# Kernel optimization log

Measured on AMD Instinct MI355X. Metric: run time of the kernel, lower is better.

The kernel has to match this reference:

```python
import jax, jax.numpy as jnp
import numpy as np

BATCH, SEQ, D_IN, D_ST = 16, 8192, 64, 128  # in_features=64, out_features(state)=128


def setup_inputs() -> dict:
    key = jax.random.key(0)
    k0, k1, k2, k3 = jax.random.split(key, 4)
    x = jax.random.normal(k0, (BATCH, SEQ, D_IN), dtype=jnp.float32)
    # State-transition matrix A (HiPPO-initialized in the original). We draw a
    # random dense matrix scaled to spectral radius ~0.9 so the 8192-step
    # recurrence stays numerically stable.
    A = jax.random.normal(k1, (D_ST, D_ST), dtype=jnp.float32) * (0.9 / np.sqrt(D_ST))
    Bw = jax.random.normal(k2, (D_ST, D_IN), dtype=jnp.float32) / np.sqrt(D_IN)
    Bb = jnp.zeros((D_ST,), dtype=jnp.float32)  # bias=True on B
    Cw = jax.random.normal(k3, (D_IN, D_ST), dtype=jnp.float32) / np.sqrt(D_ST)
    return {"x": x, "A": A, "Bw": Bw, "Bb": Bb, "Cw": Cw}


def reference(x, A, Bw, Bb, Cw):
    # Discrete linear SSM: h_t = A h_{t-1} + (B x_t + b),  y_t = C h_t
    # Input projection is batched into one big GEMM (not per-step).
    bx = jnp.einsum('bsi,di->bsd', x, Bw) + Bb          # [B,S,D_ST]
    bx_t = jnp.transpose(bx, (1, 0, 2))                  # [S,B,D_ST]

    def step(h, u):
        h = u + h @ A.T                                  # [B,D_ST]
        return h, h

    h0 = jnp.zeros((x.shape[0], A.shape[0]), dtype=x.dtype)
    _, hs = jax.lax.scan(step, h0, bx_t)                 # hs: [S,B,D_ST]
    # Output projection as one big GEMM after the scan.
    y = jnp.einsum('sbd,od->bso', hs, Cw)                # [B,S,D_IN]
    return y
```

## Files before the change

kernel.cpp:

```cpp
#include <hip/hip_runtime.h>


#define SEQ   8192
#define DIN   64
#define LCH   16
#define NCH   (SEQ / LCH)
#define KCOMB 7

typedef _Float16 v8h __attribute__((ext_vector_type(8)));
typedef __fp16   v2h __attribute__((ext_vector_type(2)));
typedef float    v4f __attribute__((ext_vector_type(4)));

#define MFMA(a, b, c) __builtin_amdgcn_mfma_f32_16x16x32_f16((a), (b), (c), 0, 0, 0)
#define PKRTZ __builtin_amdgcn_cvt_pkrtz
#define Z4 (v4f{0.f, 0.f, 0.f, 0.f})

#define OFF_AH 0
#define OFF_AL 16384
#define OFF_BH 32768
#define OFF_BL 40960
#define OFF_CH 49152
#define OFF_CL 57344
#define OFF_TH 65536
#define OFF_TL 81920

__device__ __forceinline__ void block_sync() {
  asm volatile("s_waitcnt lgkmcnt(0)" ::: "memory");
  __builtin_amdgcn_s_barrier();
  asm volatile("" ::: "memory");
}

__device__ __forceinline__ int rho_fwd(int lidx) {
  int kt = lidx >> 5, q = (lidx >> 3) & 3, e = lidx & 7;
  int eh = e >> 1;
  int m = kt + 4 * (eh & 1);
  int r = 2 * (eh >> 1) + (e & 1);
  return 16 * m + 4 * q + r;
}
__device__ __forceinline__ int rho_inv(int p) {
  int m = p >> 4, q = (p >> 2) & 3, r = p & 3;
  int eh = ((r >> 1) << 1) | (m >> 2);
  int e  = (eh << 1) | (r & 1);
  return 32 * (m & 3) + 8 * q + e;
}
__device__ __forceinline__ void pack_hl(float v, _Float16* hp, _Float16* lp) {
  _Float16 h = (_Float16)v;
  *hp = h; *lp = (_Float16)(v - (float)h);
}

__global__ void mmk(const float* __restrict__ X, const float* __restrict__ Y,
                    float* __restrict__ D) {
  int idx = blockIdx.x * 256 + threadIdx.x;
  int i = idx >> 7, j = idx & 127;
  const float* xr = X + i * 128;
  const float* yc = Y + j;
  float s0 = 0.f, s1 = 0.f, s2 = 0.f, s3 = 0.f;
#pragma unroll
  for (int k = 0; k < 128; k += 4) {
    s0 = fmaf(xr[k],     yc[(k)     * 128], s0);
    s1 = fmaf(xr[k + 1], yc[(k + 1) * 128], s1);
    s2 = fmaf(xr[k + 2], yc[(k + 2) * 128], s2);
    s3 = fmaf(xr[k + 3], yc[(k + 3) * 128], s3);
  }
  D[idx] = (s0 + s1) + (s2 + s3);
}

__global__ void packk(const float* __restrict__ A, const float* __restrict__ Bw,
                      const float* __restrict__ Bb, const float* __restrict__ Cw,
                      const float* __restrict__ A8, _Float16* __restrict__ F,
                      float* __restrict__ Bbs) {
  int idx = blockIdx.x * 256 + threadIdx.x;
  if (idx < 16384) {
    int i = idx >> 7, j = idx & 127;
    int o = rho_fwd(i) * 128 + j;
    pack_hl(A[idx], F + OFF_AH + o, F + OFF_AL + o);
  } else if (idx < 24576) {
    int p = idx - 16384; int i = p >> 6, j = p & 63;
    int o = rho_fwd(i) * 64 + j;
    pack_hl(Bw[p], F + OFF_BH + o, F + OFF_BL + o);
  } else if (idx < 32768) {
    int p = idx - 24576;
    pack_hl(Cw[p], F + OFF_CH + p, F + OFF_CL + p);
  } else if (idx < 32896) {
    int i = idx - 32768;
    Bbs[i] = Bb[rho_inv(i)];
  } else if (idx < 49280) {
    int p = idx - 32896; int i = p >> 7, j = p & 127;
    const float* xr = A8 + i * 128;
    const float* yc = A8 + j;
    float s0 = 0.f, s1 = 0.f, s2 = 0.f, s3 = 0.f;
#pragma unroll
    for (int k = 0; k < 128; k += 4) {
      s0 = fmaf(xr[k],     yc[(k)     * 128], s0);
      s1 = fmaf(xr[k + 1], yc[(k + 1) * 128], s1);
      s2 = fmaf(xr[k + 2], yc[(k + 2) * 128], s2);
      s3 = fmaf(xr[k + 3], yc[(k + 3) * 128], s3);
    }
    float v = (s0 + s1) + (s2 + s3);
    int o = rho_fwd(i) * 128 + j;
    pack_hl(v, F + OFF_TH + o, F + OFF_TL + o);
  }
}

__device__ __forceinline__ void split16(const v4f* b, v8h& xh0, v8h& xh1,
                                        v8h& xl0, v8h& xl1) {
  union { v2h h2[4]; v8h h8; } H0, H1;
  H0.h2[0] = PKRTZ(b[0][0], b[0][1]); H0.h2[1] = PKRTZ(b[0][2], b[0][3]);
  H0.h2[2] = PKRTZ(b[1][0], b[1][1]); H0.h2[3] = PKRTZ(b[1][2], b[1][3]);
  H1.h2[0] = PKRTZ(b[2][0], b[2][1]); H1.h2[1] = PKRTZ(b[2][2], b[2][3]);
  H1.h2[2] = PKRTZ(b[3][0], b[3][1]); H1.h2[3] = PKRTZ(b[3][2], b[3][3]);
  float r[16];
#pragma unroll
  for (int i = 0; i < 8; ++i) r[i]     = b[i >> 2][i & 3]       - (float)H0.h8[i];
#pragma unroll
  for (int i = 0; i < 8; ++i) r[8 + i] = b[2 + (i >> 2)][i & 3] - (float)H1.h8[i];
  union { v2h h2[4]; v8h h8; } L0, L1;
  L0.h2[0] = PKRTZ(r[0], r[1]);   L0.h2[1] = PKRTZ(r[2], r[3]);
  L0.h2[2] = PKRTZ(r[4], r[5]);   L0.h2[3] = PKRTZ(r[6], r[7]);
  L1.h2[0] = PKRTZ(r[8], r[9]);   L1.h2[1] = PKRTZ(r[10], r[11]);
  L1.h2[2] = PKRTZ(r[12], r[13]); L1.h2[3] = PKRTZ(r[14], r[15]);
  xh0 = H0.h8; xh1 = H1.h8; xl0 = L0.h8; xl1 = L1.h8;
}

__global__ __launch_bounds__(256, 2) void scan1(
    const float* __restrict__ x, const _Float16* __restrict__ F,
    const float* __restrict__ Bbs, float* __restrict__ Vbuf) {
  const int tid = threadIdx.x;
  const int wv  = tid >> 6;
  const int l   = tid & 63;
  const int n   = l & 15;
  const int q   = l >> 4;
  const int c   = blockIdx.x;
  const int t0  = c * LCH;

  v8h afh[2][4], afl[2][4], bwh[2][2], bwl[2][2];
  v4f bb2[2];
#pragma unroll
  for (int i = 0; i < 2; ++i) {
    int row = 16 * (wv + 4 * i) + n;
#pragma unroll
    for (int kt = 0; kt < 4; ++kt) {
      afh[i][kt] = *(const v8h*)(F + OFF_AH + row * 128 + 32 * kt + 8 * q);
      afl[i][kt] = *(const v8h*)(F + OFF_AL + row * 128 + 32 * kt + 8 * q);
    }
#pragma unroll
    for (int k2 = 0; k2 < 2; ++k2) {
      bwh[i][k2] = *(const v8h*)(F + OFF_BH + row * 64 + 32 * k2 + 8 * q);
      bwl[i][k2] = *(const v8h*)(F + OFF_BL + row * 64 + 32 * k2 + 8 * q);
    }
    bb2[i] = *(const v4f*)(Bbs + 16 * (wv + 4 * i) + 4 * q);
  }

  __shared__ _Float16 hx[2][2][4][512];

  const float* xb = x + (size_t)n * (SEQ * DIN) + 8 * q;
  v4f bufA[4], bufB[4], uA[2], uB[2];
  auto loadx = [&](v4f(&buf)[4], int t) {
    const float* p = xb + (size_t)t * DIN;
    buf[0] = *(const v4f*)(p);      buf[1] = *(const v4f*)(p + 4);
    buf[2] = *(const v4f*)(p + 32); buf[3] = *(const v4f*)(p + 36);
  };
  auto build_u = [&](const v4f(&b)[4]) {
    v8h xh0, xh1, xl0, xl1;
    split16(b, xh0, xh1, xl0, xl1);
#pragma unroll
    for (int i = 0; i < 2; ++i) {
      v4f a = bb2[i];
      a = MFMA(bwh[i][0], xh0, a);
      a = MFMA(bwh[i][1], xh1, a);
      uA[i] = a;
      v4f b1 = MFMA(bwl[i][0], xh0, Z4);
      b1 = MFMA(bwl[i][1], xh1, b1);
      v4f b2 = MFMA(bwh[i][0], xl0, Z4);
      b2 = MFMA(bwh[i][1], xl1, b2);
      uB[i] = b1 + b2;
    }
  };
  auto xwrite = [&](int pr, const v4f& a0, const v4f& a1) {
    union { v2h h2[4]; v8h h8; } U;
    U.h2[0] = PKRTZ(a0[0], a0[1]); U.h2[1] = PKRTZ(a1[0], a1[1]);
    U.h2[2] = PKRTZ(a0[2], a0[3]); U.h2[3] = PKRTZ(a1[2], a1[3]);
    *(v8h*)&hx[pr][0][wv][l * 8] = U.h8;
    float r0 = a0[0] - (float)U.h8[0], r1 = a0[1] - (float)U.h8[1];
    float r2 = a1[0] - (float)U.h8[2], r3 = a1[1] - (float)U.h8[3];
    float r4 = a0[2] - (float)U.h8[4], r5 = a0[3] - (float)U.h8[5];
    float r6 = a1[2] - (float)U.h8[6], r7 = a1[3] - (float)U.h8[7];
    union { v2h h2[4]; v8h h8; } L;
    L.h2[0] = PKRTZ(r0, r1); L.h2[1] = PKRTZ(r2, r3);
    L.h2[2] = PKRTZ(r4, r5); L.h2[3] = PKRTZ(r6, r7);
    *(v8h*)&hx[pr][1][wv][l * 8] = L.h8;
  };

  v8h hf[4], hlo[4];
#pragma unroll
  for (int kt = 0; kt < 4; ++kt) { hf[kt] = v8h{}; hlo[kt] = v8h{}; }

  auto rec24 = [&](v4f(&acc)[2]) {
#pragma unroll
    for (int i = 0; i < 2; ++i) {
      v4f a = MFMA(afh[i][0], hf[0], uA[i]);
      a     = MFMA(afh[i][1], hf[1], a);
      v4f b = MFMA(afh[i][2], hf[2], Z4);
      b     = MFMA(afh[i][3], hf[3], b);
      v4f c2a = MFMA(afl[i][0], hf[0], uB[i]);
      c2a     = MFMA(afl[i][1], hf[1], c2a);
      v4f c2b = MFMA(afl[i][2], hf[2], Z4);
      c2b     = MFMA(afl[i][3], hf[3], c2b);
      v4f c3a = MFMA(afh[i][0], hlo[0], Z4);
      c3a     = MFMA(afh[i][1], hlo[1], c3a);
      v4f c3b = MFMA(afh[i][2], hlo[2], Z4);
      c3b     = MFMA(afh[i][3], hlo[3], c3b);
      acc[i] = (a + b) + (c2a + c2b) + (c3a + c3b);
    }
  };

  auto step = [&](int t, v4f(&bsrc)[4], v4f(&bld)[4], int pr) {
    int tn = t + 2; if (tn > SEQ - 1) tn = SEQ - 1;
    loadx(bld, tn);
    v4f acc[2];
    rec24(acc);
    xwrite(pr, acc[0], acc[1]);
    block_sync();
    build_u(bsrc);
#pragma unroll
    for (int kt = 0; kt < 4; ++kt) {
      hf[kt]  = *(const v8h*)&hx[pr][0][kt][l * 8];
      hlo[kt] = *(const v8h*)&hx[pr][1][kt][l * 8];
    }
  };

  loadx(bufA, t0);
  loadx(bufB, t0 + 1);
  build_u(bufA);
#pragma unroll
  for (int tp = 0; tp < 7; ++tp) {
    step(t0 + 2 * tp,     bufB, bufA, 0);
    step(t0 + 2 * tp + 1, bufA, bufB, 1);
  }
  step(t0 + 14, bufB, bufA, 0);
  v4f acc[2];
  rec24(acc);
  float* vb = Vbuf + (size_t)c * 2048 + tid * 8;
  *(v4f*)vb       = acc[0];
  *(v4f*)(vb + 4) = acc[1];
}

__global__ __launch_bounds__(256, 2) void scan2(
    const float* __restrict__ x, float* __restrict__ y,
    const _Float16* __restrict__ F, const float* __restrict__ Bbs,
    const float* __restrict__ Vbuf) {
  const int tid = threadIdx.x;
  const int wv  = tid >> 6;
  const int l   = tid & 63;
  const int n   = l & 15;
  const int q   = l >> 4;
  const int c   = blockIdx.x;
  const int t0  = c * LCH, te = t0 + LCH;

  __shared__ _Float16 hx[2][2][4][512];

  const float* xb = x + (size_t)n * (SEQ * DIN) + 8 * q;
  float* yb = y + (size_t)n * (SEQ * DIN);
  v4f bufA[4], bufB[4];
  auto loadx = [&](v4f(&buf)[4], int t) {
    const float* p = xb + (size_t)t * DIN;
    buf[0] = *(const v4f*)(p);      buf[1] = *(const v4f*)(p + 4);
    buf[2] = *(const v4f*)(p + 32); buf[3] = *(const v4f*)(p + 36);
  };
  loadx(bufA, t0);
  loadx(bufB, t0 + 1);

  v8h afh[2][4], afl[2][4];
  auto load_AF = [&](int oh, int ol) {
#pragma unroll
    for (int i = 0; i < 2; ++i) {
      int row = 16 * (wv + 4 * i) + n;
#pragma unroll
      for (int kt = 0; kt < 4; ++kt) {
        afh[i][kt] = *(const v8h*)(F + oh + row * 128 + 32 * kt + 8 * q);
        afl[i][kt] = *(const v8h*)(F + ol + row * 128 + 32 * kt + 8 * q);
      }
    }
  };

  auto xwrite = [&](int pr, const v4f& a0, const v4f& a1) {
    union { v2h h2[4]; v8h h8; } U;
    U.h2[0] = PKRTZ(a0[0], a0[1]); U.h2[1] = PKRTZ(a1[0], a1[1]);
    U.h2[2] = PKRTZ(a0[2], a0[3]); U.h2[3] = PKRTZ(a1[2], a1[3]);
    *(v8h*)&hx[pr][0][wv][l * 8] = U.h8;
    float r0 = a0[0] - (float)U.h8[0], r1 = a0[1] - (float)U.h8[1];
    float r2 = a1[0] - (float)U.h8[2], r3 = a1[1] - (float)U.h8[3];
    float r4 = a0[2] - (float)U.h8[4], r5 = a0[3] - (float)U.h8[5];
    float r6 = a1[2] - (float)U.h8[6], r7 = a1[3] - (float)U.h8[7];
    union { v2h h2[4]; v8h h8; } L;
    L.h2[0] = PKRTZ(r0, r1); L.h2[1] = PKRTZ(r2, r3);
    L.h2[2] = PKRTZ(r4, r5); L.h2[3] = PKRTZ(r6, r7);
    *(v8h*)&hx[pr][1][wv][l * 8] = L.h8;
  };

  v8h hf[4], hlo[4];
#pragma unroll
  for (int kt = 0; kt < 4; ++kt) { hf[kt] = v8h{}; hlo[kt] = v8h{}; }

  int pr = 0;

  if (c > 0) {
    load_AF(OFF_TH, OFF_TL);
    const int kmax = (c < KCOMB) ? c : KCOMB;
    const float* vp = Vbuf + (size_t)(c - kmax) * 2048 + tid * 8;
    v4f v0 = *(const v4f*)vp, v1 = *(const v4f*)(vp + 4);
    for (int kk = kmax; kk >= 1; --kk) {
      v4f vc0 = v0, vc1 = v1;
      if (kk > 1) {
        const float* vn = Vbuf + (size_t)(c - kk + 1) * 2048 + tid * 8;
        v0 = *(const v4f*)vn; v1 = *(const v4f*)(vn + 4);
      }
      v4f acc[2];
#pragma unroll
      for (int i = 0; i < 2; ++i) {
        v4f ui = (i == 0) ? vc0 : vc1;
        v4f a = MFMA(afh[i][0], hf[0], ui);
        a     = MFMA(afh[i][1], hf[1], a);
        v4f b = MFMA(afh[i][2], hf[2], Z4);
        b     = MFMA(afh[i][3], hf[3], b);
        v4f c2a = MFMA(afl[i][0], hf[0], Z4);
        c2a     = MFMA(afl[i][1], hf[1], c2a);
        v4f c2b = MFMA(afl[i][2], hf[2], Z4);
        c2b     = MFMA(afl[i][3], hf[3], c2b);
        v4f c3a = MFMA(afh[i][0], hlo[0], Z4);
        c3a     = MFMA(afh[i][1], hlo[1], c3a);
        v4f c3b = MFMA(afh[i][2], hlo[2], Z4);
        c3b     = MFMA(afh[i][3], hlo[3], c3b);
        acc[i] = (a + b) + (c2a + c2b) + (c3a + c3b);
      }
      xwrite(pr, acc[0], acc[1]);
      block_sync();
#pragma unroll
      for (int kt = 0; kt < 4; ++kt) {
        hf[kt]  = *(const v8h*)&hx[pr][0][kt][l * 8];
        hlo[kt] = *(const v8h*)&hx[pr][1][kt][l * 8];
      }
      pr ^= 1;
    }
  }
  load_AF(OFF_AH, OFF_AL);

  v8h bwh[2][2], bwl[2][2], cwh[4], cwl[4];
  v4f bb2[2];
#pragma unroll
  for (int i = 0; i < 2; ++i) {
    int row = 16 * (wv + 4 * i) + n;
#pragma unroll
    for (int k2 = 0; k2 < 2; ++k2) {
      bwh[i][k2] = *(const v8h*)(F + OFF_BH + row * 64 + 32 * k2 + 8 * q);
      bwl[i][k2] = *(const v8h*)(F + OFF_BL + row * 64 + 32 * k2 + 8 * q);
    }
    bb2[i] = *(const v4f*)(Bbs + 16 * (wv + 4 * i) + 4 * q);
  }
  {
    int row = 16 * wv + n;
#pragma unroll
    for (int kt = 0; kt < 4; ++kt) {
      cwh[kt] = *(const v8h*)(F + OFF_CH + row * 128 + 32 * kt + 8 * q);
      cwl[kt] = *(const v8h*)(F + OFF_CL + row * 128 + 32 * kt + 8 * q);
    }
  }

  v4f uA[2], uB[2];
  auto build_u = [&](const v4f(&b)[4]) {
    v8h xh0, xh1, xl0, xl1;
    split16(b, xh0, xh1, xl0, xl1);
#pragma unroll
    for (int i = 0; i < 2; ++i) {
      v4f a = bb2[i];
      a = MFMA(bwh[i][0], xh0, a);
      a = MFMA(bwh[i][1], xh1, a);
      uA[i] = a;
      v4f b1 = MFMA(bwl[i][0], xh0, Z4);
      b1 = MFMA(bwl[i][1], xh1, b1);
      v4f b2 = MFMA(bwh[i][0], xl0, Z4);
      b2 = MFMA(bwh[i][1], xl1, b2);
      uB[i] = b1 + b2;
    }
  };
  auto emit_y = [&](int t) {
    v4f e1a = MFMA(cwh[1], hf[1], MFMA(cwh[0], hf[0], Z4));
    v4f e1b = MFMA(cwh[3], hf[3], MFMA(cwh[2], hf[2], Z4));
    v4f e2a = MFMA(cwh[1], hlo[1], MFMA(cwh[0], hlo[0], Z4));
    v4f e2b = MFMA(cwh[3], hlo[3], MFMA(cwh[2], hlo[2], Z4));
    v4f e3a = MFMA(cwl[1], hf[1], MFMA(cwl[0], hf[0], Z4));
    v4f e3b = MFMA(cwl[3], hf[3], MFMA(cwl[2], hf[2], Z4));
    v4f r = (e1a + e1b) + (e2a + e2b) + (e3a + e3b);
    *(v4f*)(yb + (size_t)t * DIN + 16 * wv + 4 * q) = r;
  };
  auto stepE = [&](int t, v4f(&bsrc)[4], v4f(&bld)[4], bool emit) {
    int tn = t + 2; if (tn > SEQ - 1) tn = SEQ - 1;
    loadx(bld, tn);
    if (emit) emit_y(t - 1);
    v4f acc[2];
#pragma unroll
    for (int i = 0; i < 2; ++i) {
      v4f a = MFMA(afh[i][0], hf[0], uA[i]);
      a     = MFMA(afh[i][1], hf[1], a);
      v4f b = MFMA(afh[i][2], hf[2], Z4);
      b     = MFMA(afh[i][3], hf[3], b);
      v4f c2a = MFMA(afl[i][0], hf[0], uB[i]);
      c2a     = MFMA(afl[i][1], hf[1], c2a);
      v4f c2b = MFMA(afl[i][2], hf[2], Z4);
      c2b     = MFMA(afl[i][3], hf[3], c2b);
      v4f c3a = MFMA(afh[i][0], hlo[0], Z4);
      c3a     = MFMA(afh[i][1], hlo[1], c3a);
      v4f c3b = MFMA(afh[i][2], hlo[2], Z4);
      c3b     = MFMA(afh[i][3], hlo[3], c3b);
      acc[i] = (a + b) + (c2a + c2b) + (c3a + c3b);
    }
    xwrite(pr, acc[0], acc[1]);
    block_sync();
    build_u(bsrc);
#pragma unroll
    for (int kt = 0; kt < 4; ++kt) {
      hf[kt]  = *(const v8h*)&hx[pr][0][kt][l * 8];
      hlo[kt] = *(const v8h*)&hx[pr][1][kt][l * 8];
    }
    pr ^= 1;
  };

  build_u(bufA);
#pragma unroll
  for (int tp = 0; tp < 8; ++tp) {
    stepE(t0 + 2 * tp,     bufB, bufA, tp > 0);
    stepE(t0 + 2 * tp + 1, bufA, bufB, true);
  }
  emit_y(te - 1);
}

extern "C" void kernel_launch(void* const* d_in, const int* in_sizes, int n_in,
                              void* d_out, int out_size, void* d_ws, size_t ws_size,
                              hipStream_t stream) {
  const float* x  = (const float*)d_in[0];
  const float* A  = (const float*)d_in[1];
  const float* Bw = (const float*)d_in[2];
  const float* Bb = (const float*)d_in[3];
  const float* Cw = (const float*)d_in[4];
  float* y = (float*)d_out;

  _Float16* F    = (_Float16*)d_ws;
  float*    Bbs  = (float*)((char*)d_ws + 196608);
  float*    pw   = (float*)((char*)d_ws + 197120);
  float*    Vbuf = (float*)((char*)d_ws + 393728);

  float* A2 = pw;
  float* A4 = pw + 16384;
  float* A8 = pw + 32768;

  mmk<<<64, 256, 0, stream>>>(A,  A,  A2);
  mmk<<<64, 256, 0, stream>>>(A2, A2, A4);
  mmk<<<64, 256, 0, stream>>>(A4, A4, A8);
  packk<<<193, 256, 0, stream>>>(A, Bw, Bb, Cw, A8, F, Bbs);
  scan1<<<NCH, 256, 0, stream>>>(x, F, Bbs, Vbuf);
  scan2<<<NCH, 256, 0, stream>>>(x, y, F, Bbs, Vbuf);
}
```

Before: 90.66 us.

## Emit local outputs in scan1 and apply carry correction via precomputed C·A^k

scan1 now computes y for each chunk from a zero initial state and stores its final chunk state in fp16 hi/lo form. scan2 no longer redoes the 16-step recurrence. It combines the incoming carry from up to seven previous chunks using the A^16, A^32 and A^64 powers in a tree, then adds C·A^(j+1)·carry to the stored y rows. Precomputing more matrix powers and the Cw·A^k products adds extra small GEMM launches plus a larger pack kernel. It also changes the workspace layout, with VbufB placed over the pw region.

Result: slower. 120.9 us (+33.4%).

```diff
diff --git a/kernel.cpp b/kernel.cpp
--- a/kernel.cpp
+++ b/kernel.cpp
@@ -15,14 +15,20 @@
 #define PKRTZ __builtin_amdgcn_cvt_pkrtz
 #define Z4 (v4f{0.f, 0.f, 0.f, 0.f})
 
-#define OFF_AH 0
-#define OFF_AL 16384
-#define OFF_BH 32768
-#define OFF_BL 40960
-#define OFF_CH 49152
-#define OFF_CL 57344
-#define OFF_TH 65536
-#define OFF_TL 81920
+#define OFF_AH   0
+#define OFF_AL   16384
+#define OFF_BH   32768
+#define OFF_BL   40960
+#define OFF_CH   49152
+#define OFF_CL   57344
+#define OFF_TH   65536
+#define OFF_TL   81920
+#define OFF_T2H  98304
+#define OFF_T2L  114688
+#define OFF_T4H  131072
+#define OFF_T4L  147456
+#define OFF_GH   163840
+#define OFF_GL   294912
 
 __device__ __forceinline__ void block_sync() {
   asm volatile("s_waitcnt lgkmcnt(0)" ::: "memory");
@@ -48,9 +54,29 @@
   *hp = h; *lp = (_Float16)(v - (float)h);
 }
 
-__global__ void mmk(const float* __restrict__ X, const float* __restrict__ Y,
-                    float* __restrict__ D) {
-  int idx = blockIdx.x * 256 + threadIdx.x;
+__global__ void mm(const float* __restrict__ A, const float* __restrict__ Cw,
+                   float* __restrict__ pw, int level) {
+  static const int tab[5][9][4] = {
+    {{-2,-1,81920,64},{-1,-1,0,128},{0,0,0,0},{0,0,0,0},{0,0,0,0},{0,0,0,0},{0,0,0,0},{0,0,0,0},{0,0,0,0}},
+    {{-2,0,90112,64},{81920,0,98304,64},{0,0,16384,128},{0,0,0,0},{0,0,0,0},{0,0,0,0},{0,0,0,0},{0,0,0,0},{0,0,0,0}},
+    {{-2,16384,106496,64},{81920,16384,114688,64},{90112,16384,122880,64},{98304,16384,131072,64},{16384,16384,32768,128},{0,0,0,0},{0,0,0,0},{0,0,0,0},{0,0,0,0}},
+    {{-2,32768,139264,64},{81920,32768,147456,64},{90112,32768,155648,64},{98304,32768,163840,64},{106496,32768,172032,64},{114688,32768,180224,64},{122880,32768,188416,64},{131072,32768,196608,64},{32768,32768,49152,128}},
+    {{-2,49152,204800,64},{49152,49152,65536,128},{0,0,0,0},{0,0,0,0},{0,0,0,0},{0,0,0,0},{0,0,0,0},{0,0,0,0},{0,0,0,0}}
+  };
+  static const int cnt[5] = {2, 3, 5, 9, 2};
+  int b = blockIdx.x;
+  int sx = 0, sy = 0, dst = 0, rows = 0;
+  for (int k = 0; k < cnt[level]; ++k) {
+    int nb = tab[level][k][3] >> 1;
+    if (b < nb) { sx = tab[level][k][0]; sy = tab[level][k][1];
+                  dst = tab[level][k][2]; rows = tab[level][k][3]; break; }
+    b -= nb;
+  }
+  if (rows == 0) return;
+  const float* X = (sx == -2) ? Cw : ((sx == -1) ? A : pw + sx);
+  const float* Y = (sy == -1) ? A : pw + sy;
+  float* D = pw + dst;
+  int idx = b * 256 + threadIdx.x;
   int i = idx >> 7, j = idx & 127;
   const float* xr = X + i * 128;
   const float* yc = Y + j;
@@ -67,7 +93,7 @@
 
 __global__ void packk(const float* __restrict__ A, const float* __restrict__ Bw,
                       const float* __restrict__ Bb, const float* __restrict__ Cw,
-                      const float* __restrict__ A8, _Float16* __restrict__ F,
+                      const float* __restrict__ pw, _Float16* __restrict__ F,
                       float* __restrict__ Bbs) {
   int idx = blockIdx.x * 256 + threadIdx.x;
   if (idx < 16384) {
@@ -85,9 +111,17 @@
     int i = idx - 32768;
     Bbs[i] = Bb[rho_inv(i)];
   } else if (idx < 49280) {
-    int p = idx - 32896; int i = p >> 7, j = p & 127;
-    const float* xr = A8 + i * 128;
-    const float* yc = A8 + j;
+    int r = idx - 32896; int i = r >> 7, j = r & 127;
+    int o = rho_fwd(i) * 128 + j;
+    pack_hl(pw[49152 + r], F + OFF_TH + o, F + OFF_TL + o);
+  } else if (idx < 65664) {
+    int r = idx - 49280; int i = r >> 7, j = r & 127;
+    int o = rho_fwd(i) * 128 + j;
+    pack_hl(pw[65536 + r], F + OFF_T2H + o, F + OFF_T2L + o);
+  } else if (idx < 82048) {
+    int r = idx - 65664; int i = r >> 7, j = r & 127;
+    const float* xr = pw + 65536 + i * 128;
+    const float* yc = pw + 65536 + j;
     float s0 = 0.f, s1 = 0.f, s2 = 0.f, s3 = 0.f;
 #pragma unroll
     for (int k = 0; k < 128; k += 4) {
@@ -98,7 +132,12 @@
     }
     float v = (s0 + s1) + (s2 + s3);
     int o = rho_fwd(i) * 128 + j;
-    pack_hl(v, F + OFF_TH + o, F + OFF_TL + o);
+    pack_hl(v, F + OFF_T4H + o, F + OFF_T4L + o);
+  } else if (idx < 213120) {
+    int p = idx - 82048;
+    int jj = p >> 13, r = p & 8191;
+    pack_hl(pw[81920 + jj * 8192 + r],
+            F + OFF_GH + jj * 8192 + r, F + OFF_GL + jj * 8192 + r);
   }
 }
 
@@ -123,17 +162,18 @@
 }
 
 __global__ __launch_bounds__(256, 2) void scan1(
-    const float* __restrict__ x, const _Float16* __restrict__ F,
-    const float* __restrict__ Bbs, float* __restrict__ Vbuf) {
+    const float* __restrict__ x, float* __restrict__ y,
+    const _Float16* __restrict__ F, const float* __restrict__ Bbs,
+    _Float16* __restrict__ VbufB) {
   const int tid = threadIdx.x;
   const int wv  = tid >> 6;
   const int l   = tid & 63;
   const int n   = l & 15;
   const int q   = l >> 4;
   const int c   = blockIdx.x;
-  const int t0  = c * LCH;
-
-  v8h afh[2][4], afl[2][4], bwh[2][2], bwl[2][2];
+  const int t0  = c * LCH, te = t0 + LCH;
+
+  v8h afh[2][4], afl[2][4], bwh[2][2], bwl[2][2], cwh[4], cwl[4];
   v4f bb2[2];
 #pragma unroll
   for (int i = 0; i < 2; ++i) {
@@ -150,10 +190,19 @@
     }
     bb2[i] = *(const v4f*)(Bbs + 16 * (wv + 4 * i) + 4 * q);
   }
+  {
+    int row = 16 * wv + n;
+#pragma unroll
+    for (int kt = 0; kt < 4; ++kt) {
+      cwh[kt] = *(const v8h*)(F + OFF_CH + row * 128 + 32 * kt + 8 * q);
+      cwl[kt] = *(const v8h*)(F + OFF_CL + row * 128 + 32 * kt + 8 * q);
+    }
+  }
 
   __shared__ _Float16 hx[2][2][4][512];
 
   const float* xb = x + (size_t)n * (SEQ * DIN) + 8 * q;
+  float* yb = y + (size_t)n * (SEQ * DIN);
   v4f bufA[4], bufB[4], uA[2], uB[2];
   auto loadx = [&](v4f(&buf)[4], int t) {
     const float* p = xb + (size_t)t * DIN;
@@ -195,7 +244,22 @@
 #pragma unroll
   for (int kt = 0; kt < 4; ++kt) { hf[kt] = v8h{}; hlo[kt] = v8h{}; }
 
-  auto rec24 = [&](v4f(&acc)[2]) {
+  auto emit_y = [&](int t) {
+    v4f e1a = MFMA(cwh[1], hf[1], MFMA(cwh[0], hf[0], Z4));
+    v4f e1b = MFMA(cwh[3], hf[3], MFMA(cwh[2], hf[2], Z4));
+    v4f e2a = MFMA(cwh[1], hlo[1], MFMA(cwh[0], hlo[0], Z4));
+    v4f e2b = MFMA(cwh[3], hlo[3], MFMA(cwh[2], hlo[2], Z4));
+    v4f e3a = MFMA(cwl[1], hf[1], MFMA(cwl[0], hf[0], Z4));
+    v4f e3b = MFMA(cwl[3], hf[3], MFMA(cwl[2], hf[2], Z4));
+    v4f r = (e1a + e1b) + (e2a + e2b) + (e3a + e3b);
+    *(v4f*)(yb + (size_t)t * DIN + 16 * wv + 4 * q) = r;
+  };
+
+  auto stepE = [&](int t, v4f(&bsrc)[4], v4f(&bld)[4], int pr, bool emit) {
+    int tn = t + 2; if (tn > SEQ - 1) tn = SEQ - 1;
+    loadx(bld, tn);
+    if (emit) emit_y(t - 1);
+    v4f acc[2];
 #pragma unroll
     for (int i = 0; i < 2; ++i) {
       v4f a = MFMA(afh[i][0], hf[0], uA[i]);
@@ -212,13 +276,6 @@
       c3b     = MFMA(afh[i][3], hlo[3], c3b);
       acc[i] = (a + b) + (c2a + c2b) + (c3a + c3b);
     }
-  };
-
-  auto step = [&](int t, v4f(&bsrc)[4], v4f(&bld)[4], int pr) {
-    int tn = t + 2; if (tn > SEQ - 1) tn = SEQ - 1;
-    loadx(bld, tn);
-    v4f acc[2];
-    rec24(acc);
     xwrite(pr, acc[0], acc[1]);
     block_sync();
     build_u(bsrc);
@@ -233,61 +290,101 @@
   loadx(bufB, t0 + 1);
   build_u(bufA);
 #pragma unroll
-  for (int tp = 0; tp < 7; ++tp) {
-    step(t0 + 2 * tp,     bufB, bufA, 0);
-    step(t0 + 2 * tp + 1, bufA, bufB, 1);
-  }
-  step(t0 + 14, bufB, bufA, 0);
-  v4f acc[2];
-  rec24(acc);
-  float* vb = Vbuf + (size_t)c * 2048 + tid * 8;
-  *(v4f*)vb       = acc[0];
-  *(v4f*)(vb + 4) = acc[1];
+  for (int tp = 0; tp < 8; ++tp) {
+    stepE(t0 + 2 * tp,     bufB, bufA, 0, tp > 0);
+    stepE(t0 + 2 * tp + 1, bufA, bufB, 1, true);
+  }
+  emit_y(te - 1);
+  _Float16* vb = VbufB + (size_t)c * 4096;
+#pragma unroll
+  for (int kt = 0; kt < 4; ++kt) {
+    *(v8h*)(vb + kt * 512 + l * 8)        = hf[kt];
+    *(v8h*)(vb + 2048 + kt * 512 + l * 8) = hlo[kt];
+  }
 }
 
 __global__ __launch_bounds__(256, 2) void scan2(
-    const float* __restrict__ x, float* __restrict__ y,
-    const _Float16* __restrict__ F, const float* __restrict__ Bbs,
-    const float* __restrict__ Vbuf) {
+    float* __restrict__ y, const _Float16* __restrict__ F,
+    const _Float16* __restrict__ VbufB) {
   const int tid = threadIdx.x;
   const int wv  = tid >> 6;
   const int l   = tid & 63;
   const int n   = l & 15;
   const int q   = l >> 4;
   const int c   = blockIdx.x;
-  const int t0  = c * LCH, te = t0 + LCH;
-
-  __shared__ _Float16 hx[2][2][4][512];
-
-  const float* xb = x + (size_t)n * (SEQ * DIN) + 8 * q;
-  float* yb = y + (size_t)n * (SEQ * DIN);
-  v4f bufA[4], bufB[4];
-  auto loadx = [&](v4f(&buf)[4], int t) {
-    const float* p = xb + (size_t)t * DIN;
-    buf[0] = *(const v4f*)(p);      buf[1] = *(const v4f*)(p + 4);
-    buf[2] = *(const v4f*)(p + 32); buf[3] = *(const v4f*)(p + 36);
-  };
-  loadx(bufA, t0);
-  loadx(bufB, t0 + 1);
-
-  v8h afh[2][4], afl[2][4];
-  auto load_AF = [&](int oh, int ol) {
+  const int t0  = c * LCH;
+  if (c == 0) return;
+
+  __shared__ _Float16 hx3[3][2][4][512];
+
+  int offD[2][4];
+#pragma unroll
+  for (int i = 0; i < 2; ++i)
+#pragma unroll
+    for (int r = 0; r < 4; ++r) {
+      int p = 16 * (wv + 4 * i) + 4 * q + r;
+      int s = rho_inv(p);
+      int kt = s >> 5, qt = (s >> 3) & 3, e = s & 7;
+      offD[i][r] = kt * 512 + (qt * 16 + n) * 8 + e;
+    }
+  auto gatherD = [&](int k, v4f(&d)[2]) {
+    if (k > c) { d[0] = Z4; d[1] = Z4; return; }
+    const _Float16* vb = VbufB + (size_t)(c - k) * 4096;
+#pragma unroll
+    for (int i = 0; i < 2; ++i)
+#pragma unroll
+      for (int r = 0; r < 4; ++r)
+        d[i][r] = (float)vb[offD[i][r]] + (float)vb[2048 + offD[i][r]];
+  };
+  auto gatherB = [&](int k, v8h(&vh)[4], v8h(&vl)[4]) {
+    if (k > c) {
+#pragma unroll
+      for (int kt = 0; kt < 4; ++kt) { vh[kt] = v8h{}; vl[kt] = v8h{}; }
+      return;
+    }
+    const _Float16* vb = VbufB + (size_t)(c - k) * 4096;
+#pragma unroll
+    for (int kt = 0; kt < 4; ++kt) {
+      vh[kt] = *(const v8h*)(vb + kt * 512 + l * 8);
+      vl[kt] = *(const v8h*)(vb + 2048 + kt * 512 + l * 8);
+    }
+  };
+
+  v8h mh[2][4], ml[2][4];
+  auto load_MAT = [&](int oh, int ol) {
 #pragma unroll
     for (int i = 0; i < 2; ++i) {
       int row = 16 * (wv + 4 * i) + n;
 #pragma unroll
       for (int kt = 0; kt < 4; ++kt) {
-        afh[i][kt] = *(const v8h*)(F + oh + row * 128 + 32 * kt + 8 * q);
-        afl[i][kt] = *(const v8h*)(F + ol + row * 128 + 32 * kt + 8 * q);
+        mh[i][kt] = *(const v8h*)(F + oh + row * 128 + 32 * kt + 8 * q);
+        ml[i][kt] = *(const v8h*)(F + ol + row * 128 + 32 * kt + 8 * q);
       }
     }
   };
-
-  auto xwrite = [&](int pr, const v4f& a0, const v4f& a1) {
+  auto prod3 = [&](const v8h(&vh)[4], const v8h(&vl)[4], v4f(&acc)[2]) {
+#pragma unroll
+    for (int i = 0; i < 2; ++i) {
+      v4f a = MFMA(mh[i][0], vh[0], acc[i]);
+      a     = MFMA(mh[i][1], vh[1], a);
+      v4f b = MFMA(mh[i][2], vh[2], Z4);
+      b     = MFMA(mh[i][3], vh[3], b);
+      v4f c2a = MFMA(ml[i][0], vh[0], Z4);
+      c2a     = MFMA(ml[i][1], vh[1], c2a);
+      v4f c2b = MFMA(ml[i][2], vh[2], Z4);
+      c2b     = MFMA(ml[i][3], vh[3], c2b);
+      v4f c3a = MFMA(mh[i][0], vl[0], Z4);
+      c3a     = MFMA(mh[i][1], vl[1], c3a);
+      v4f c3b = MFMA(mh[i][2], vl[2], Z4);
+      c3b     = MFMA(mh[i][3], vl[3], c3b);
+      acc[i] = (a + b) + (c2a + c2b) + (c3a + c3b);
+    }
+  };
+  auto xwrite3 = [&](int sl, const v4f& a0, const v4f& a1) {
     union { v2h h2[4]; v8h h8; } U;
     U.h2[0] = PKRTZ(a0[0], a0[1]); U.h2[1] = PKRTZ(a1[0], a1[1]);
     U.h2[2] = PKRTZ(a0[2], a0[3]); U.h2[3] = PKRTZ(a1[2], a1[3]);
-    *(v8h*)&hx[pr][0][wv][l * 8] = U.h8;
+    *(v8h*)&hx3[sl][0][wv][l * 8] = U.h8;
     float r0 = a0[0] - (float)U.h8[0], r1 = a0[1] - (float)U.h8[1];
     float r2 = a1[0] - (float)U.h8[2], r3 = a1[1] - (float)U.h8[3];
     float r4 = a0[2] - (float)U.h8[4], r5 = a0[3] - (float)U.h8[5];
@@ -295,143 +392,54 @@
     union { v2h h2[4]; v8h h8; } L;
     L.h2[0] = PKRTZ(r0, r1); L.h2[1] = PKRTZ(r2, r3);
     L.h2[2] = PKRTZ(r4, r5); L.h2[3] = PKRTZ(r6, r7);
-    *(v8h*)&hx[pr][1][wv][l * 8] = L.h8;
-  };
-
+    *(v8h*)&hx3[sl][1][wv][l * 8] = L.h8;
+  };
+  auto readB3 = [&](int sl, v8h(&vh)[4], v8h(&vl)[4]) {
+#pragma unroll
+    for (int kt = 0; kt < 4; ++kt) {
+      vh[kt] = *(const v8h*)&hx3[sl][0][kt][l * 8];
+      vl[kt] = *(const v8h*)&hx3[sl][1][kt][l * 8];
+    }
+  };
+
+  v4f wa[2], wb[2], wd[2];
+  v8h vh[4], vl[4];
+  load_MAT(OFF_TH, OFF_TL);
+  gatherD(1, wa); gatherB(2, vh, vl); prod3(vh, vl, wa);
+  gatherD(3, wb); gatherB(4, vh, vl); prod3(vh, vl, wb);
+  gatherD(5, wd); gatherB(6, vh, vl); prod3(vh, vl, wd);
+  load_MAT(OFF_T2H, OFF_T2L);
+  gatherB(7, vh, vl); prod3(vh, vl, wd);
+  xwrite3(0, wb[0], wb[1]);
+  xwrite3(1, wd[0], wd[1]);
+  block_sync();
+  readB3(0, vh, vl); prod3(vh, vl, wa);
+  load_MAT(OFF_T4H, OFF_T4L);
+  readB3(1, vh, vl); prod3(vh, vl, wa);
+  xwrite3(2, wa[0], wa[1]);
+  block_sync();
   v8h hf[4], hlo[4];
-#pragma unroll
-  for (int kt = 0; kt < 4; ++kt) { hf[kt] = v8h{}; hlo[kt] = v8h{}; }
-
-  int pr = 0;
-
-  if (c > 0) {
-    load_AF(OFF_TH, OFF_TL);
-    const int kmax = (c < KCOMB) ? c : KCOMB;
-    const float* vp = Vbuf + (size_t)(c - kmax) * 2048 + tid * 8;
-    v4f v0 = *(const v4f*)vp, v1 = *(const v4f*)(vp + 4);
-    for (int kk = kmax; kk >= 1; --kk) {
-      v4f vc0 = v0, vc1 = v1;
-      if (kk > 1) {
-        const float* vn = Vbuf + (size_t)(c - kk + 1) * 2048 + tid * 8;
-        v0 = *(const v4f*)vn; v1 = *(const v4f*)(vn + 4);
-      }
-      v4f acc[2];
-#pragma unroll
-      for (int i = 0; i < 2; ++i) {
-        v4f ui = (i == 0) ? vc0 : vc1;
-        v4f a = MFMA(afh[i][0], hf[0], ui);
-        a     = MFMA(afh[i][1], hf[1], a);
-        v4f b = MFMA(afh[i][2], hf[2], Z4);
-        b     = MFMA(afh[i][3], hf[3], b);
-        v4f c2a = MFMA(afl[i][0], hf[0], Z4);
-        c2a     = MFMA(afl[i][1], hf[1], c2a);
-        v4f c2b = MFMA(afl[i][2], hf[2], Z4);
-        c2b     = MFMA(afl[i][3], hf[3], c2b);
-        v4f c3a = MFMA(afh[i][0], hlo[0], Z4);
-        c3a     = MFMA(afh[i][1], hlo[1], c3a);
-        v4f c3b = MFMA(afh[i][2], hlo[2], Z4);
-        c3b     = MFMA(afh[i][3], hlo[3], c3b);
-        acc[i] = (a + b) + (c2a + c2b) + (c3a + c3b);
-      }
-      xwrite(pr, acc[0], acc[1]);
-      block_sync();
-#pragma unroll
-      for (int kt = 0; kt < 4; ++kt) {
-        hf[kt]  = *(const v8h*)&hx[pr][0][kt][l * 8];
-        hlo[kt] = *(const v8h*)&hx[pr][1][kt][l * 8];
-      }
-      pr ^= 1;
-    }
-  }
-  load_AF(OFF_AH, OFF_AL);
-
-  v8h bwh[2][2], bwl[2][2], cwh[4], cwl[4];
-  v4f bb2[2];
-#pragma unroll
-  for (int i = 0; i < 2; ++i) {
-    int row = 16 * (wv + 4 * i) + n;
-#pragma unroll
-    for (int k2 = 0; k2 < 2; ++k2) {
-      bwh[i][k2] = *(const v8h*)(F + OFF_BH + row * 64 + 32 * k2 + 8 * q);
-      bwl[i][k2] = *(const v8h*)(F + OFF_BL + row * 64 + 32 * k2 + 8 * q);
-    }
-    bb2[i] = *(const v4f*)(Bbs + 16 * (wv + 4 * i) + 4 * q);
-  }
-  {
-    int row = 16 * wv + n;
-#pragma unroll
-    for (int kt = 0; kt < 4; ++kt) {
-      cwh[kt] = *(const v8h*)(F + OFF_CH + row * 128 + 32 * kt + 8 * q);
-      cwl[kt] = *(const v8h*)(F + OFF_CL + row * 128 + 32 * kt + 8 * q);
-    }
-  }
-
-  v4f uA[2], uB[2];
-  auto build_u = [&](const v4f(&b)[4]) {
-    v8h xh0, xh1, xl0, xl1;
-    split16(b, xh0, xh1, xl0, xl1);
-#pragma unroll
-    for (int i = 0; i < 2; ++i) {
-      v4f a = bb2[i];
-      a = MFMA(bwh[i][0], xh0, a);
-      a = MFMA(bwh[i][1], xh1, a);
-      uA[i] = a;
-      v4f b1 = MFMA(bwl[i][0], xh0, Z4);
-      b1 = MFMA(bwl[i][1], xh1, b1);
-      v4f b2 = MFMA(bwh[i][0], xl0, Z4);
-      b2 = MFMA(bwh[i][1], xl1, b2);
-      uB[i] = b1 + b2;
-    }
-  };
-  auto emit_y = [&](int t) {
-    v4f e1a = MFMA(cwh[1], hf[1], MFMA(cwh[0], hf[0], Z4));
-    v4f e1b = MFMA(cwh[3], hf[3], MFMA(cwh[2], hf[2], Z4));
-    v4f e2a = MFMA(cwh[1], hlo[1], MFMA(cwh[0], hlo[0], Z4));
-    v4f e2b = MFMA(cwh[3], hlo[3], MFMA(cwh[2], hlo[2], Z4));
-    v4f e3a = MFMA(cwl[1], hf[1], MFMA(cwl[0], hf[0], Z4));
-    v4f e3b = MFMA(cwl[3], hf[3], MFMA(cwl[2], hf[2], Z4));
-    v4f r = (e1a + e1b) + (e2a + e2b) + (e3a + e3b);
-    *(v4f*)(yb + (size_t)t * DIN + 16 * wv + 4 * q) = r;
-  };
-  auto stepE = [&](int t, v4f(&bsrc)[4], v4f(&bld)[4], bool emit) {
-    int tn = t + 2; if (tn > SEQ - 1) tn = SEQ - 1;
-    loadx(bld, tn);
-    if (emit) emit_y(t - 1);
-    v4f acc[2];
-#pragma unroll
-    for (int i = 0; i < 2; ++i) {
-      v4f a = MFMA(afh[i][0], hf[0], uA[i]);
-      a     = MFMA(afh[i][1], hf[1], a);
-      v4f b = MFMA(afh[i][2], hf[2], Z4);
-      b     = MFMA(afh[i][3], hf[3], b);
-      v4f c2a = MFMA(afl[i][0], hf[0], uB[i]);
-      c2a     = MFMA(afl[i][1], hf[1], c2a);
-      v4f c2b = MFMA(afl[i][2], hf[2], Z4);
-      c2b     = MFMA(afl[i][3], hf[3], c2b);
-      v4f c3a = MFMA(afh[i][0], hlo[0], Z4);
-      c3a     = MFMA(afh[i][1], hlo[1], c3a);
-      v4f c3b = MFMA(afh[i][2], hlo[2], Z4);
-      c3b     = MFMA(afh[i][3], hlo[3], c3b);
-      acc[i] = (a + b) + (c2a + c2b) + (c3a + c3b);
-    }
-    xwrite(pr, acc[0], acc[1]);
-    block_sync();
-    build_u(bsrc);
-#pragma unroll
-    for (int kt = 0; kt < 4; ++kt) {
-      hf[kt]  = *(const v8h*)&hx[pr][0][kt][l * 8];
-      hlo[kt] = *(const v8h*)&hx[pr][1][kt][l * 8];
-    }
-    pr ^= 1;
-  };
-
-  build_u(bufA);
-#pragma unroll
-  for (int tp = 0; tp < 8; ++tp) {
-    stepE(t0 + 2 * tp,     bufB, bufA, tp > 0);
-    stepE(t0 + 2 * tp + 1, bufA, bufB, true);
-  }
-  emit_y(te - 1);
+  readB3(2, hf, hlo);
+
+  float* yb = y + (size_t)n * (SEQ * DIN);
+  const int grow = 16 * wv + n;
+  for (int j = 0; j < 16; ++j) {
+    v8h gh[4], gl[4];
+#pragma unroll
+    for (int kt = 0; kt < 4; ++kt) {
+      gh[kt] = *(const v8h*)(F + OFF_GH + j * 8192 + grow * 128 + 32 * kt + 8 * q);
+      gl[kt] = *(const v8h*)(F + OFF_GL + j * 8192 + grow * 128 + 32 * kt + 8 * q);
+    }
+    v4f e1a = MFMA(gh[1], hf[1], MFMA(gh[0], hf[0], Z4));
+    v4f e1b = MFMA(gh[3], hf[3], MFMA(gh[2], hf[2], Z4));
+    v4f e2a = MFMA(gh[1], hlo[1], MFMA(gh[0], hlo[0], Z4));
+    v4f e2b = MFMA(gh[3], hlo[3], MFMA(gh[2], hlo[2], Z4));
+    v4f e3a = MFMA(gl[1], hf[1], MFMA(gl[0], hf[0], Z4));
+    v4f e3b = MFMA(gl[3], hf[3], MFMA(gl[2], hf[2], Z4));
+    v4f corr = (e1a + e1b) + (e2a + e2b) + (e3a + e3b);
+    float* yp = yb + (size_t)(t0 + j) * DIN + 16 * wv + 4 * q;
+    *(v4f*)yp = *(const v4f*)yp + corr;
+  }
 }
 
 extern "C" void kernel_launch(void* const* d_in, const int* in_sizes, int n_in,
@@ -444,19 +452,17 @@
   const float* Cw = (const float*)d_in[4];
   float* y = (float*)d_out;
 
-  _Float16* F    = (_Float16*)d_ws;
-  float*    Bbs  = (float*)((char*)d_ws + 196608);
-  float*    pw   = (float*)((char*)d_ws + 197120);
-  float*    Vbuf = (float*)((char*)d_ws + 393728);
-
-  float* A2 = pw;
-  float* A4 = pw + 16384;
-  float* A8 = pw + 32768;
-
-  mmk<<<64, 256, 0, stream>>>(A,  A,  A2);
-  mmk<<<64, 256, 0, stream>>>(A2, A2, A4);
-  mmk<<<64, 256, 0, stream>>>(A4, A4, A8);
-  packk<<<193, 256, 0, stream>>>(A, Bw, Bb, Cw, A8, F, Bbs);
-  scan1<<<NCH, 256, 0, stream>>>(x, F, Bbs, Vbuf);
-  scan2<<<NCH, 256, 0, stream>>>(x, y, F, Bbs, Vbuf);
-}
+  _Float16* F     = (_Float16*)d_ws;
+  float*    Bbs   = (float*)((char*)d_ws + 851968);
+  float*    pw    = (float*)((char*)d_ws + 852480);
+  _Float16* VbufB = (_Float16*)((char*)d_ws + 852480);
+
+  mm<<<96,  256, 0, stream>>>(A, Cw, pw, 0);
+  mm<<<128, 256, 0, stream>>>(A, Cw, pw, 1);
+  mm<<<192, 256, 0, stream>>>(A, Cw, pw, 2);
+  mm<<<320, 256, 0, stream>>>(A, Cw, pw, 3);
+  mm<<<96,  256, 0, stream>>>(A, Cw, pw, 4);
+  packk<<<833, 256, 0, stream>>>(A, Bw, Bb, Cw, pw, F, Bbs);
+  scan1<<<NCH, 256, 0, stream>>>(x, y, F, Bbs, VbufB);
+  scan2<<<NCH, 256, 0, stream>>>(y, F, VbufB);
+}
```
